# Optimization experiments

Measured on AMD Instinct MI355X. Metric: run time of the kernel, lower is better.

The kernel has to match this reference:

```python
import jax, jax.numpy as jnp
import numpy as np

CUTOFF = 5.2
BUCKETS_PER_CUTOFF = 1
BOX = 100.0
N_ATOMS = 100000
EXTRA_SPACE = 1e-5

# half-shell neighbor displacements: cartesian_prod(arange(-b,1)^3)[:-1] -> 7 vectors for b=1
_d1 = np.arange(-BUCKETS_PER_CUTOFF, 1)
DISPLACEMENTS = jnp.asarray(
    np.stack(np.meshgrid(_d1, _d1, _d1, indexing='ij'), axis=-1).reshape(-1, 3)[:-1],
    dtype=jnp.int32)  # (7, 3)
NUM_NEIGHBORS = DISPLACEMENTS.shape[0]


def setup_inputs() -> dict:
    key = jax.random.key(0)
    k1, _ = jax.random.split(key)
    # uniform in [0, 0.999*BOX) so fractional coordinates are strictly < 1
    coordinates = jax.random.uniform(k1, (1, N_ATOMS, 3), dtype=jnp.float32) * (BOX * 0.999)
    cell = jnp.eye(3, dtype=jnp.float32) * BOX
    return {"coordinates": coordinates, "cell": cell}


def _cumsum_from_zero(x):
    return jnp.concatenate([jnp.zeros((1,), x.dtype), jnp.cumsum(x[:-1])])


def reference(coordinates, cell):
    n_atoms = coordinates.shape[1]
    cell_diag = jnp.diagonal(cell)                       # (3,)
    bucket_length = CUTOFF / BUCKETS_PER_CUTOFF + EXTRA_SPACE
    grid = jnp.floor(cell_diag / bucket_length).astype(jnp.int32) + 1   # shape_buckets_grid (3,)
    total_buckets = int(grid[0] * grid[1] * grid[2])
    # faithful to source: [g1*g2, g1, 1]
    scaling = jnp.array([grid[1] * grid[2], grid[1], 1], dtype=jnp.int32)

    # fractionalize + main bucket vector/flat indices
    frac = coordinates / cell_diag.reshape(1, 1, -1)     # (1, N, 3)
    vec_idx = jnp.round(frac * (grid - 1).astype(frac.dtype)).astype(jnp.int32)  # (1, N, 3)
    flat = (vec_idx * scaling).sum(-1).reshape(-1)       # (N,) main_bucket_flat_index

    # image-index converters (stable argsort by bucket)
    imidx_from_atidx = jnp.argsort(flat)                 # jax argsort is stable
    atidx_from_imidx = jnp.argsort(imidx_from_atidx)

    # per-bucket counts / exclusive cumcounts
    counts = jnp.bincount(flat, length=total_buckets)
    cumcounts = _cumsum_from_zero(counts)
    max_in_bucket = int(counts.max())

    # ---- within-image pairs ----
    wp_idx = jnp.nonzero(counts > 1)[0]
    wp_count = counts[wp_idx]
    wp_cum = cumcounts[wp_idx]
    pu, pl = jnp.triu_indices(max_in_bucket, k=1)
    pairs = jnp.stack([pu, pl]).astype(jnp.int32)        # (2, P)
    # sort_along_row(row_for_sorting=1): key = upper + lower*max_in_bucket
    order = jnp.argsort(pairs[0] + pairs[1] * max_in_bucket)
    pairs = pairs[:, order]
    padded = pairs[None] + wp_cum.reshape(-1, 1, 1)      # (B, 2, P)
    padded = jnp.transpose(padded, (1, 0, 2)).reshape(2, -1)
    max_pairs = max_in_bucket * (max_in_bucket - 1) // 2
    mask = (jnp.arange(max_pairs)[None, :] < (wp_count * (wp_count - 1) // 2)[:, None]).reshape(-1)
    within_image_pairs = jnp.stack([padded[0][mask], padded[1][mask]])  # (2, n_pairs)

    # ---- between-image 'lower' indices ----
    neigh_vec = vec_idx[:, :, None, :] + DISPLACEMENTS   # (1, N, 7, 3)
    neigh_vec = jnp.mod(neigh_vec, grid)                 # pbc wrap of neighbor buckets
    neigh_flat = (neigh_vec * scaling).sum(-1)           # (1, N, 7)
    n_count = counts[neigh_flat]                         # (1, N, 7)
    n_cum = cumcounts[neigh_flat]                        # (1, N, 7)
    pad = jnp.broadcast_to(
        jnp.arange(max_in_bucket, dtype=n_cum.dtype).reshape(1, 1, 1, -1),
        (1, n_atoms, NUM_NEIGHBORS, max_in_bucket))      # (1, N, 7, M) -- dominant intermediate
    m = pad < n_count[..., None]
    lower_between = (pad + n_cum[..., None])[m]          # (n_between,)

    return within_image_pairs, lower_between, frac, imidx_from_atidx, atidx_from_imidx
```

## Files before the change

kernel.cpp:

```cpp
#include <hip/hip_runtime.h>
#include <hip/hip_bf16.h>

#define NB_MAX 8192
#define NTHR 256

__device__ __forceinline__ void get_grid(const float* __restrict__ cell,
                                         int& g0, int& g1, int& g2,
                                         float& d0, float& d1, float& d2) {
  d0 = cell[0]; d1 = cell[4]; d2 = cell[8];
  const float bl = (float)(5.2 + 1e-05);
  g0 = (int)floorf(d0 / bl) + 1;
  g1 = (int)floorf(d1 / bl) + 1;
  g2 = (int)floorf(d2 / bl) + 1;
}

__global__ void k_bucket_count(const float* __restrict__ coord,
                               const float* __restrict__ cell,
                               float* __restrict__ out_frac,
                               int* __restrict__ flat,
                               int* __restrict__ pv,
                               int* __restrict__ counts,
                               int* __restrict__ scalars, int n) {
  int a = blockIdx.x * blockDim.x + threadIdx.x;
  if (a >= n) return;
  int g0, g1, g2; float d0, d1, d2;
  get_grid(cell, g0, g1, g2, d0, d1, d2);
  if (a == 0) {
    scalars[8] = g0; scalars[9] = g1; scalars[10] = g2;
    scalars[11] = g1 * g2; scalars[12] = g0 * g1 * g2;
  }
  float x = coord[3 * a + 0], y = coord[3 * a + 1], z = coord[3 * a + 2];
  float fx = x / d0, fy = y / d1, fz = z / d2;
  out_frac[3 * a + 0] = fx;
  out_frac[3 * a + 1] = fy;
  out_frac[3 * a + 2] = fz;
  int v0 = (int)rintf(fx * (float)(g0 - 1));
  int v1 = (int)rintf(fy * (float)(g1 - 1));
  int v2 = (int)rintf(fz * (float)(g2 - 1));
  int b = v0 * (g1 * g2) + v1 * g1 + v2;
  flat[a] = b;
  pv[a] = (v0 << 20) | (v1 << 10) | v2;
  atomicAdd(&counts[b], 1);
}

__global__ __launch_bounds__(1024) void k_scan_buckets(
    const int* __restrict__ counts,
    int* __restrict__ cumc,
    int* __restrict__ pairoff,
    int* __restrict__ scalars) {
  int nb = scalars[12];
  const int T = 1024, IT = NB_MAX / 1024;
  __shared__ int wc[16], wp[16];
  int t = threadIdx.x;
  int lane = t & 63, wid = t >> 6;
  int base = t * IT;
  int cv[IT];
  int lc = 0, lp = 0;
  for (int i = 0; i < IT; ++i) {
    int idx = base + i;
    int c = (idx < nb) ? counts[idx] : 0;
    cv[i] = c;
    lc += c;
    lp += c * (c - 1) / 2;
  }
  int ic = lc, ip = lp;
  for (int off = 1; off < 64; off <<= 1) {
    int yc = __shfl_up(ic, off);
    int yp = __shfl_up(ip, off);
    if (lane >= off) { ic += yc; ip += yp; }
  }
  if (lane == 63) { wc[wid] = ic; wp[wid] = ip; }
  __syncthreads();
  if (wid == 0 && lane < 16) {
    int vc2 = wc[lane], vp2 = wp[lane];
    int sc2 = vc2, sp2 = vp2;
    for (int off = 1; off < 16; off <<= 1) {
      int yc = __shfl_up(sc2, off);
      int yp = __shfl_up(sp2, off);
      if (lane >= off) { sc2 += yc; sp2 += yp; }
    }
    wc[lane] = sc2 - vc2;
    wp[lane] = sp2 - vp2;
  }
  __syncthreads();
  int ec = wc[wid] + (ic - lc);
  int ep = wp[wid] + (ip - lp);
  for (int i = 0; i < IT; ++i) {
    int idx = base + i;
    if (idx < nb) { cumc[idx] = ec; pairoff[idx] = ep; }
    ec += cv[i];
    ep += cv[i] * (cv[i] - 1) / 2;
  }
  if (t == T - 1) scalars[0] = ep;
}

__global__ void k_scatter_runlen(const int* __restrict__ flat,
                                 const int* __restrict__ pv,
                                 const int* __restrict__ cumc,
                                 const int* __restrict__ counts,
                                 const int* __restrict__ scalars,
                                 int* __restrict__ fill,
                                 int* __restrict__ sorted,
                                 int* __restrict__ Oarr,
                                 int* __restrict__ blockpart, int n) {
  __shared__ int ws[4];
  int t = threadIdx.x;
  int lane = t & 63, wid = t >> 6;
  int a = blockIdx.x * NTHR + t;
  int S = 0;
  if (a < n) {
    int b = flat[a];
    int pos = cumc[b] + atomicAdd(&fill[b], 1);
    sorted[pos] = a;
    int g0 = scalars[8], g1 = scalars[9], g2 = scalars[10], g12 = scalars[11];
    int p = pv[a];
    int v0 = p >> 20, v1 = (p >> 10) & 1023, v2 = p & 1023;
#pragma unroll
    for (int m = 0; m < 7; ++m) {
      int dx = ((m >> 2) & 1) ? 0 : -1;
      int dy = ((m >> 1) & 1) ? 0 : -1;
      int dz = (m & 1) ? 0 : -1;
      int nx = v0 + dx; if (nx < 0) nx += g0;
      int ny = v1 + dy; if (ny < 0) ny += g1;
      int nz = v2 + dz; if (nz < 0) nz += g2;
      S += counts[nx * g12 + ny * g1 + nz];
    }
  }
  int iv = S;
  for (int off = 1; off < 64; off <<= 1) {
    int y = __shfl_up(iv, off);
    if (lane >= off) iv += y;
  }
  if (lane == 63) ws[wid] = iv;
  __syncthreads();
  if (wid == 0 && lane < 4) {
    int v2 = ws[lane], s2 = v2;
    for (int off = 1; off < 4; off <<= 1) {
      int y = __shfl_up(s2, off);
      if (lane >= off) s2 += y;
    }
    ws[lane] = s2 - v2;
    if (lane == 3) blockpart[blockIdx.x] = s2;
  }
  __syncthreads();
  if (a < n) Oarr[a] = ws[wid] + (iv - S);
}

__global__ void k_sort_perm_pairs(const int* __restrict__ counts,
                                  const int* __restrict__ cumc,
                                  const int* __restrict__ pairoff,
                                  const int* __restrict__ scalars,
                                  int* __restrict__ sorted,
                                  float* __restrict__ out_im,
                                  float* __restrict__ out_at,
                                  float* __restrict__ out,
                                  const int* __restrict__ blockpart,
                                  int* __restrict__ blockoff, int nblocks) {
  __shared__ int shm[4];
  int t = threadIdx.x;
  int lane = t & 63, wid = t >> 6;
  if (blockIdx.x == gridDim.x - 1) {
    int base = t * 4;
    int cv[4];
    int ls = 0;
    for (int i = 0; i < 4; ++i) {
      int v = (base + i < nblocks) ? blockpart[base + i] : 0;
      cv[i] = v;
      ls += v;
    }
    int il = ls;
    for (int off = 1; off < 64; off <<= 1) {
      int y = __shfl_up(il, off);
      if (lane >= off) il += y;
    }
    if (lane == 63) shm[wid] = il;
    __syncthreads();
    if (wid == 0 && lane < 4) {
      int v2 = shm[lane], s2 = v2;
      for (int off = 1; off < 4; off <<= 1) {
        int y = __shfl_up(s2, off);
        if (lane >= off) s2 += y;
      }
      shm[lane] = s2 - v2;
    }
    __syncthreads();
    int e = shm[wid] + (il - ls);
    for (int i = 0; i < 4; ++i) {
      blockoff[base + i] = e;
      e += cv[i];
    }
    return;
  }
  int b = blockIdx.x * 4 + wid;
  int nb = scalars[12];
  if (b >= nb) return;
  int c = counts[b];
  if (c == 0) return;
  int s = cumc[b];
  if (c == 1) {
    if (lane == 0) {
      int a = sorted[s];
      out_im[s] = (float)a;
      out_at[a] = (float)s;
    }
    return;
  }
  if (c <= 64) {
    int val = (lane < c) ? sorted[s + lane] : 0x7fffffff;
    int rank = 0;
    for (int j = 0; j < c; ++j) {
      int other = __shfl(val, j);
      rank += (other < val) ? 1 : 0;
    }
    if (lane < c) {
      sorted[s + rank] = val;
      out_im[s + rank] = (float)val;
      out_at[val] = (float)(s + rank);
    }
  } else if (lane == 0) {
    for (int i = 1; i < c; ++i) {
      int key = sorted[s + i];
      int j = i - 1;
      while (j >= 0 && sorted[s + j] > key) {
        sorted[s + j + 1] = sorted[s + j];
        --j;
      }
      sorted[s + j + 1] = key;
    }
    for (int i = 0; i < c; ++i) {
      int a = sorted[s + i];
      out_im[s + i] = (float)a;
      out_at[a] = (float)(s + i);
    }
  }
  int off = pairoff[b];
  int P = scalars[0];
  int np = c * (c - 1) / 2;
  for (int k = lane; k < np; k += 64) {
    int l = (int)((1.0f + sqrtf(1.0f + 8.0f * (float)k)) * 0.5f);
    while (l * (l - 1) / 2 > k) --l;
    while ((l + 1) * l / 2 <= k) ++l;
    int u = k - l * (l - 1) / 2;
    out[off + k] = (float)(s + u);
    out[P + off + k] = (float)(s + l);
  }
}

__global__ void k_emit16(const int* __restrict__ pv,
                         const int* __restrict__ counts,
                         const int* __restrict__ cumc,
                         const int* __restrict__ Oarr,
                         const int* __restrict__ blockoff,
                         const int* __restrict__ scalars,
                         float* __restrict__ out, int n) {
  int gt = blockIdx.x * blockDim.x + threadIdx.x;
  int a = gt >> 4;
  int l16 = gt & 15;
  if (a >= n) return;
  int g0 = scalars[8], g1 = scalars[9], g2 = scalars[10], g12 = scalars[11];
  int p = pv[a];
  int v0 = p >> 20, v1 = (p >> 10) & 1023, v2 = p & 1023;
  int segs[8];
  int cums[7];
  segs[0] = 0;
#pragma unroll
  for (int m = 0; m < 7; ++m) {
    int dx = ((m >> 2) & 1) ? 0 : -1;
    int dy = ((m >> 1) & 1) ? 0 : -1;
    int dz = (m & 1) ? 0 : -1;
    int nx = v0 + dx; if (nx < 0) nx += g0;
    int ny = v1 + dy; if (ny < 0) ny += g1;
    int nz = v2 + dz; if (nz < 0) nz += g2;
    int nb_ = nx * g12 + ny * g1 + nz;
    cums[m] = cumc[nb_];
    segs[m + 1] = segs[m] + counts[nb_];
  }
  int S = segs[7];
  long base = 2L * (long)scalars[0] + (long)blockoff[a >> 8] + (long)Oarr[a];
  for (int q = l16; q < S; q += 16) {
    int v = cums[0] + q;
#pragma unroll
    for (int m = 1; m < 7; ++m) {
      if (q >= segs[m]) v = cums[m] + (q - segs[m]);
    }
    out[base + q] = (float)v;
  }
}

extern "C" void kernel_launch(void* const* d_in, const int* in_sizes, int n_in,
                              void* d_out, int out_size, void* d_ws, size_t ws_size,
                              hipStream_t stream) {
  const float* coord = (const float*)d_in[0];
  const float* cell = (const float*)d_in[1];
  float* out = (float*)d_out;
  int n = in_sizes[0] / 3;

  int* W = (int*)d_ws;
  int* counts = W;
  int* fill = W + NB_MAX;
  int* scalars = W + 2 * NB_MAX;
  int* cumc = W + 2 * NB_MAX + 16;
  int* pairoff = cumc + NB_MAX;
  int* flat = pairoff + NB_MAX;
  int* pv = flat + n;
  int* sorted = pv + n;
  int* Oarr = sorted + n;
  int* blockpart = Oarr + n;
  int* blockoff = blockpart + 1024;

  float* out_frac = out + (out_size - 5 * n);
  float* out_im = out + (out_size - 2 * n);
  float* out_at = out + (out_size - n);

  int nblocks = (n + NTHR - 1) / NTHR;

  hipMemsetAsync(d_ws, 0, (size_t)(2 * NB_MAX + 16) * sizeof(int), stream);

  k_bucket_count<<<nblocks, NTHR, 0, stream>>>(coord, cell, out_frac, flat, pv, counts, scalars, n);
  k_scan_buckets<<<1, 1024, 0, stream>>>(counts, cumc, pairoff, scalars);
  k_scatter_runlen<<<nblocks, NTHR, 0, stream>>>(flat, pv, cumc, counts, scalars,
                                                 fill, sorted, Oarr, blockpart, n);
  k_sort_perm_pairs<<<NB_MAX / 4 + 1, 256, 0, stream>>>(counts, cumc, pairoff, scalars,
                                                        sorted, out_im, out_at, out,
                                                        blockpart, blockoff, nblocks);
  k_emit16<<<(n * 16 + 255) / 256, 256, 0, stream>>>(pv, counts, cumc, Oarr, blockoff,
                                                     scalars, out, n);
}
```

Before: 115.7 us.

## Fuse four pipeline kernels into one cooperative kernel with grid syncs

Replaces the bucket-count, bucket scan, scatter/run-length and sort/pair kernels with a single cooperative kernel that uses grid.sync between phases. The flat bucket index stays in a register instead of round-tripping through global memory, and the per-bucket sort phase becomes a grid-stride loop over warps. The aim is to remove launch overhead and inter-kernel gaps in a latency-bound pipeline. In exchange it adds grid-wide barrier cost, requires all ~391 blocks to be co-resident, and moves the bucket scan from a 1024-thread block to a single 256-thread block.

Measured after the change: 271.8 us. +135.0%, slower.

```diff
diff --git a/kernel.cpp b/kernel.cpp
--- a/kernel.cpp
+++ b/kernel.cpp
@@ -1,248 +1,227 @@
 #include <hip/hip_runtime.h>
 #include <hip/hip_bf16.h>
+#include <hip/hip_cooperative_groups.h>
+
+namespace cg = cooperative_groups;
 
 #define NB_MAX 8192
 #define NTHR 256
 
-__device__ __forceinline__ void get_grid(const float* __restrict__ cell,
-                                         int& g0, int& g1, int& g2,
-                                         float& d0, float& d1, float& d2) {
-  d0 = cell[0]; d1 = cell[4]; d2 = cell[8];
-  const float bl = (float)(5.2 + 1e-05);
-  g0 = (int)floorf(d0 / bl) + 1;
-  g1 = (int)floorf(d1 / bl) + 1;
-  g2 = (int)floorf(d2 / bl) + 1;
-}
-
-__global__ void k_bucket_count(const float* __restrict__ coord,
-                               const float* __restrict__ cell,
-                               float* __restrict__ out_frac,
-                               int* __restrict__ flat,
-                               int* __restrict__ pv,
-                               int* __restrict__ counts,
-                               int* __restrict__ scalars, int n) {
-  int a = blockIdx.x * blockDim.x + threadIdx.x;
-  if (a >= n) return;
-  int g0, g1, g2; float d0, d1, d2;
-  get_grid(cell, g0, g1, g2, d0, d1, d2);
-  if (a == 0) {
-    scalars[8] = g0; scalars[9] = g1; scalars[10] = g2;
-    scalars[11] = g1 * g2; scalars[12] = g0 * g1 * g2;
-  }
-  float x = coord[3 * a + 0], y = coord[3 * a + 1], z = coord[3 * a + 2];
-  float fx = x / d0, fy = y / d1, fz = z / d2;
-  out_frac[3 * a + 0] = fx;
-  out_frac[3 * a + 1] = fy;
-  out_frac[3 * a + 2] = fz;
-  int v0 = (int)rintf(fx * (float)(g0 - 1));
-  int v1 = (int)rintf(fy * (float)(g1 - 1));
-  int v2 = (int)rintf(fz * (float)(g2 - 1));
-  int b = v0 * (g1 * g2) + v1 * g1 + v2;
-  flat[a] = b;
-  pv[a] = (v0 << 20) | (v1 << 10) | v2;
-  atomicAdd(&counts[b], 1);
-}
-
-__global__ __launch_bounds__(1024) void k_scan_buckets(
-    const int* __restrict__ counts,
+__global__ __launch_bounds__(NTHR) void k_coop(
+    const float* __restrict__ coord,
+    const float* __restrict__ cell,
+    float* __restrict__ out_frac,
+    float* __restrict__ out_im,
+    float* __restrict__ out_at,
+    float* __restrict__ out,
+    int* __restrict__ pv,
+    int* __restrict__ counts,
+    int* __restrict__ fill,
+    int* __restrict__ scalars,
     int* __restrict__ cumc,
     int* __restrict__ pairoff,
-    int* __restrict__ scalars) {
-  int nb = scalars[12];
-  const int T = 1024, IT = NB_MAX / 1024;
-  __shared__ int wc[16], wp[16];
-  int t = threadIdx.x;
-  int lane = t & 63, wid = t >> 6;
-  int base = t * IT;
-  int cv[IT];
-  int lc = 0, lp = 0;
-  for (int i = 0; i < IT; ++i) {
-    int idx = base + i;
-    int c = (idx < nb) ? counts[idx] : 0;
-    cv[i] = c;
-    lc += c;
-    lp += c * (c - 1) / 2;
-  }
-  int ic = lc, ip = lp;
-  for (int off = 1; off < 64; off <<= 1) {
-    int yc = __shfl_up(ic, off);
-    int yp = __shfl_up(ip, off);
-    if (lane >= off) { ic += yc; ip += yp; }
-  }
-  if (lane == 63) { wc[wid] = ic; wp[wid] = ip; }
-  __syncthreads();
-  if (wid == 0 && lane < 16) {
-    int vc2 = wc[lane], vp2 = wp[lane];
-    int sc2 = vc2, sp2 = vp2;
-    for (int off = 1; off < 16; off <<= 1) {
-      int yc = __shfl_up(sc2, off);
-      int yp = __shfl_up(sp2, off);
-      if (lane >= off) { sc2 += yc; sp2 += yp; }
-    }
-    wc[lane] = sc2 - vc2;
-    wp[lane] = sp2 - vp2;
-  }
-  __syncthreads();
-  int ec = wc[wid] + (ic - lc);
-  int ep = wp[wid] + (ip - lp);
-  for (int i = 0; i < IT; ++i) {
-    int idx = base + i;
-    if (idx < nb) { cumc[idx] = ec; pairoff[idx] = ep; }
-    ec += cv[i];
-    ep += cv[i] * (cv[i] - 1) / 2;
-  }
-  if (t == T - 1) scalars[0] = ep;
-}
-
-__global__ void k_scatter_runlen(const int* __restrict__ flat,
-                                 const int* __restrict__ pv,
-                                 const int* __restrict__ cumc,
-                                 const int* __restrict__ counts,
-                                 const int* __restrict__ scalars,
-                                 int* __restrict__ fill,
-                                 int* __restrict__ sorted,
-                                 int* __restrict__ Oarr,
-                                 int* __restrict__ blockpart, int n) {
-  __shared__ int ws[4];
+    int* __restrict__ sorted,
+    int* __restrict__ Oarr,
+    int* __restrict__ blockpart,
+    int* __restrict__ blockoff,
+    int n) {
+  cg::grid_group grid = cg::this_grid();
+  __shared__ int shA[4], shB[4];
   int t = threadIdx.x;
   int lane = t & 63, wid = t >> 6;
   int a = blockIdx.x * NTHR + t;
-  int S = 0;
-  if (a < n) {
-    int b = flat[a];
-    int pos = cumc[b] + atomicAdd(&fill[b], 1);
-    sorted[pos] = a;
-    int g0 = scalars[8], g1 = scalars[9], g2 = scalars[10], g12 = scalars[11];
-    int p = pv[a];
-    int v0 = p >> 20, v1 = (p >> 10) & 1023, v2 = p & 1023;
+  bool active = a < n;
+
+  int flat_r = 0, pv_r = 0;
+  {
+    float d0 = cell[0], d1 = cell[4], d2 = cell[8];
+    const float bl = (float)(5.2 + 1e-05);
+    int g0 = (int)floorf(d0 / bl) + 1;
+    int g1 = (int)floorf(d1 / bl) + 1;
+    int g2 = (int)floorf(d2 / bl) + 1;
+    if (a == 0) {
+      scalars[8] = g0; scalars[9] = g1; scalars[10] = g2;
+      scalars[11] = g1 * g2; scalars[12] = g0 * g1 * g2;
+    }
+    if (active) {
+      float x = coord[3 * a + 0], y = coord[3 * a + 1], z = coord[3 * a + 2];
+      float fx = x / d0, fy = y / d1, fz = z / d2;
+      out_frac[3 * a + 0] = fx;
+      out_frac[3 * a + 1] = fy;
+      out_frac[3 * a + 2] = fz;
+      int v0 = (int)rintf(fx * (float)(g0 - 1));
+      int v1 = (int)rintf(fy * (float)(g1 - 1));
+      int v2 = (int)rintf(fz * (float)(g2 - 1));
+      flat_r = v0 * (g1 * g2) + v1 * g1 + v2;
+      pv_r = (v0 << 20) | (v1 << 10) | v2;
+      pv[a] = pv_r;
+      atomicAdd(&counts[flat_r], 1);
+    }
+  }
+  grid.sync();
+
+  if (blockIdx.x == 0) {
+    int nb = scalars[12];
+    const int IT = NB_MAX / NTHR;
+    int base2 = t * IT;
+    int lc = 0, lp = 0;
+    for (int i = 0; i < IT; ++i) {
+      int idx = base2 + i;
+      int c = (idx < nb) ? counts[idx] : 0;
+      lc += c;
+      lp += c * (c - 1) / 2;
+    }
+    int ic = lc, ip = lp;
+    for (int off = 1; off < 64; off <<= 1) {
+      int yc = __shfl_up(ic, off);
+      int yp = __shfl_up(ip, off);
+      if (lane >= off) { ic += yc; ip += yp; }
+    }
+    if (lane == 63) { shA[wid] = ic; shB[wid] = ip; }
+    __syncthreads();
+    if (wid == 0 && lane < 4) {
+      int vc2 = shA[lane], vp2 = shB[lane];
+      int sc2 = vc2, sp2 = vp2;
+      for (int off = 1; off < 4; off <<= 1) {
+        int yc = __shfl_up(sc2, off);
+        int yp = __shfl_up(sp2, off);
+        if (lane >= off) { sc2 += yc; sp2 += yp; }
+      }
+      shA[lane] = sc2 - vc2;
+      shB[lane] = sp2 - vp2;
+    }
+    __syncthreads();
+    int ec = shA[wid] + (ic - lc);
+    int ep = shB[wid] + (ip - lp);
+    for (int i = 0; i < IT; ++i) {
+      int idx = base2 + i;
+      int c = (idx < nb) ? counts[idx] : 0;
+      if (idx < nb) { cumc[idx] = ec; pairoff[idx] = ep; }
+      ec += c;
+      ep += c * (c - 1) / 2;
+    }
+    if (t == NTHR - 1) scalars[0] = ep;
+  }
+  grid.sync();
+
+  {
+    int S = 0;
+    if (active) {
+      int pos = cumc[flat_r] + atomicAdd(&fill[flat_r], 1);
+      sorted[pos] = a;
+      int g0 = scalars[8], g1 = scalars[9], g2 = scalars[10], g12 = scalars[11];
+      int v0 = pv_r >> 20, v1 = (pv_r >> 10) & 1023, v2 = pv_r & 1023;
 #pragma unroll
-    for (int m = 0; m < 7; ++m) {
-      int dx = ((m >> 2) & 1) ? 0 : -1;
-      int dy = ((m >> 1) & 1) ? 0 : -1;
-      int dz = (m & 1) ? 0 : -1;
-      int nx = v0 + dx; if (nx < 0) nx += g0;
-      int ny = v1 + dy; if (ny < 0) ny += g1;
-      int nz = v2 + dz; if (nz < 0) nz += g2;
-      S += counts[nx * g12 + ny * g1 + nz];
-    }
-  }
-  int iv = S;
-  for (int off = 1; off < 64; off <<= 1) {
-    int y = __shfl_up(iv, off);
-    if (lane >= off) iv += y;
-  }
-  if (lane == 63) ws[wid] = iv;
-  __syncthreads();
-  if (wid == 0 && lane < 4) {
-    int v2 = ws[lane], s2 = v2;
-    for (int off = 1; off < 4; off <<= 1) {
-      int y = __shfl_up(s2, off);
-      if (lane >= off) s2 += y;
-    }
-    ws[lane] = s2 - v2;
-    if (lane == 3) blockpart[blockIdx.x] = s2;
-  }
-  __syncthreads();
-  if (a < n) Oarr[a] = ws[wid] + (iv - S);
-}
-
-__global__ void k_sort_perm_pairs(const int* __restrict__ counts,
-                                  const int* __restrict__ cumc,
-                                  const int* __restrict__ pairoff,
-                                  const int* __restrict__ scalars,
-                                  int* __restrict__ sorted,
-                                  float* __restrict__ out_im,
-                                  float* __restrict__ out_at,
-                                  float* __restrict__ out,
-                                  const int* __restrict__ blockpart,
-                                  int* __restrict__ blockoff, int nblocks) {
-  __shared__ int shm[4];
-  int t = threadIdx.x;
-  int lane = t & 63, wid = t >> 6;
-  if (blockIdx.x == gridDim.x - 1) {
-    int base = t * 4;
-    int cv[4];
-    int ls = 0;
-    for (int i = 0; i < 4; ++i) {
-      int v = (base + i < nblocks) ? blockpart[base + i] : 0;
-      cv[i] = v;
-      ls += v;
-    }
-    int il = ls;
+      for (int m = 0; m < 7; ++m) {
+        int dx = ((m >> 2) & 1) ? 0 : -1;
+        int dy = ((m >> 1) & 1) ? 0 : -1;
+        int dz = (m & 1) ? 0 : -1;
+        int nx = v0 + dx; if (nx < 0) nx += g0;
+        int ny = v1 + dy; if (ny < 0) ny += g1;
+        int nz = v2 + dz; if (nz < 0) nz += g2;
+        S += counts[nx * g12 + ny * g1 + nz];
+      }
+    }
+    int iv = S;
     for (int off = 1; off < 64; off <<= 1) {
-      int y = __shfl_up(il, off);
-      if (lane >= off) il += y;
-    }
-    if (lane == 63) shm[wid] = il;
+      int y = __shfl_up(iv, off);
+      if (lane >= off) iv += y;
+    }
+    __syncthreads();
+    if (lane == 63) shA[wid] = iv;
     __syncthreads();
     if (wid == 0 && lane < 4) {
-      int v2 = shm[lane], s2 = v2;
+      int v2 = shA[lane], s2 = v2;
       for (int off = 1; off < 4; off <<= 1) {
         int y = __shfl_up(s2, off);
         if (lane >= off) s2 += y;
       }
-      shm[lane] = s2 - v2;
-    }
-    __syncthreads();
-    int e = shm[wid] + (il - ls);
-    for (int i = 0; i < 4; ++i) {
-      blockoff[base + i] = e;
-      e += cv[i];
-    }
-    return;
-  }
-  int b = blockIdx.x * 4 + wid;
-  int nb = scalars[12];
-  if (b >= nb) return;
-  int c = counts[b];
-  if (c == 0) return;
-  int s = cumc[b];
-  if (c == 1) {
-    if (lane == 0) {
-      int a = sorted[s];
-      out_im[s] = (float)a;
-      out_at[a] = (float)s;
-    }
-    return;
-  }
-  if (c <= 64) {
-    int val = (lane < c) ? sorted[s + lane] : 0x7fffffff;
-    int rank = 0;
-    for (int j = 0; j < c; ++j) {
-      int other = __shfl(val, j);
-      rank += (other < val) ? 1 : 0;
-    }
-    if (lane < c) {
-      sorted[s + rank] = val;
-      out_im[s + rank] = (float)val;
-      out_at[val] = (float)(s + rank);
-    }
-  } else if (lane == 0) {
-    for (int i = 1; i < c; ++i) {
-      int key = sorted[s + i];
-      int j = i - 1;
-      while (j >= 0 && sorted[s + j] > key) {
-        sorted[s + j + 1] = sorted[s + j];
-        --j;
-      }
-      sorted[s + j + 1] = key;
-    }
-    for (int i = 0; i < c; ++i) {
-      int a = sorted[s + i];
-      out_im[s + i] = (float)a;
-      out_at[a] = (float)(s + i);
-    }
-  }
-  int off = pairoff[b];
-  int P = scalars[0];
-  int np = c * (c - 1) / 2;
-  for (int k = lane; k < np; k += 64) {
-    int l = (int)((1.0f + sqrtf(1.0f + 8.0f * (float)k)) * 0.5f);
-    while (l * (l - 1) / 2 > k) --l;
-    while ((l + 1) * l / 2 <= k) ++l;
-    int u = k - l * (l - 1) / 2;
-    out[off + k] = (float)(s + u);
-    out[P + off + k] = (float)(s + l);
+      shA[lane] = s2 - v2;
+      if (lane == 3) blockpart[blockIdx.x] = s2;
+    }
+    __syncthreads();
+    if (active) Oarr[a] = shA[wid] + (iv - S);
+  }
+  grid.sync();
+
+  {
+    int gw = blockIdx.x * 4 + wid;
+    int nwaves = gridDim.x * 4;
+    int nblocks = gridDim.x;
+    if (gw == 0) {
+      int cv[7];
+      int ls = 0;
+      for (int i = 0; i < 7; ++i) {
+        int idx = lane * 7 + i;
+        int v = (idx < nblocks) ? blockpart[idx] : 0;
+        cv[i] = v;
+        ls += v;
+      }
+      int il = ls;
+      for (int off = 1; off < 64; off <<= 1) {
+        int y = __shfl_up(il, off);
+        if (lane >= off) il += y;
+      }
+      int e = il - ls;
+      for (int i = 0; i < 7; ++i) {
+        int idx = lane * 7 + i;
+        if (idx < nblocks) blockoff[idx] = e;
+        e += cv[i];
+      }
+    }
+    int nb = scalars[12];
+    int P = scalars[0];
+    for (int b = gw; b < nb; b += nwaves) {
+      int c = counts[b];
+      if (c == 0) continue;
+      int s = cumc[b];
+      if (c == 1) {
+        if (lane == 0) {
+          int aa = sorted[s];
+          out_im[s] = (float)aa;
+          out_at[aa] = (float)s;
+        }
+        continue;
+      }
+      if (c <= 64) {
+        int val = (lane < c) ? sorted[s + lane] : 0x7fffffff;
+        int rank = 0;
+        for (int j = 0; j < c; ++j) {
+          int other = __shfl(val, j);
+          rank += (other < val) ? 1 : 0;
+        }
+        if (lane < c) {
+          sorted[s + rank] = val;
+          out_im[s + rank] = (float)val;
+          out_at[val] = (float)(s + rank);
+        }
+      } else if (lane == 0) {
+        for (int i = 1; i < c; ++i) {
+          int key = sorted[s + i];
+          int j = i - 1;
+          while (j >= 0 && sorted[s + j] > key) {
+            sorted[s + j + 1] = sorted[s + j];
+            --j;
+          }
+          sorted[s + j + 1] = key;
+        }
+        for (int i = 0; i < c; ++i) {
+          int aa = sorted[s + i];
+          out_im[s + i] = (float)aa;
+          out_at[aa] = (float)(s + i);
+        }
+      }
+      int off = pairoff[b];
+      int np = c * (c - 1) / 2;
+      for (int k = lane; k < np; k += 64) {
+        int l = (int)((1.0f + sqrtf(1.0f + 8.0f * (float)k)) * 0.5f);
+        while (l * (l - 1) / 2 > k) --l;
+        while ((l + 1) * l / 2 <= k) ++l;
+        int u = k - l * (l - 1) / 2;
+        out[off + k] = (float)(s + u);
+        out[P + off + k] = (float)(s + l);
+      }
+    }
   }
 }
 
@@ -301,8 +280,7 @@
   int* scalars = W + 2 * NB_MAX;
   int* cumc = W + 2 * NB_MAX + 16;
   int* pairoff = cumc + NB_MAX;
-  int* flat = pairoff + NB_MAX;
-  int* pv = flat + n;
+  int* pv = pairoff + NB_MAX;
   int* sorted = pv + n;
   int* Oarr = sorted + n;
   int* blockpart = Oarr + n;
@@ -316,13 +294,14 @@
 
   hipMemsetAsync(d_ws, 0, (size_t)(2 * NB_MAX + 16) * sizeof(int), stream);
 
-  k_bucket_count<<<nblocks, NTHR, 0, stream>>>(coord, cell, out_frac, flat, pv, counts, scalars, n);
-  k_scan_buckets<<<1, 1024, 0, stream>>>(counts, cumc, pairoff, scalars);
-  k_scatter_runlen<<<nblocks, NTHR, 0, stream>>>(flat, pv, cumc, counts, scalars,
-                                                 fill, sorted, Oarr, blockpart, n);
-  k_sort_perm_pairs<<<NB_MAX / 4 + 1, 256, 0, stream>>>(counts, cumc, pairoff, scalars,
-                                                        sorted, out_im, out_at, out,
-                                                        blockpart, blockoff, nblocks);
+  void* kargs[] = {
+      (void*)&coord, (void*)&cell, (void*)&out_frac, (void*)&out_im,
+      (void*)&out_at, (void*)&out, (void*)&pv, (void*)&counts,
+      (void*)&fill, (void*)&scalars, (void*)&cumc, (void*)&pairoff,
+      (void*)&sorted, (void*)&Oarr, (void*)&blockpart, (void*)&blockoff,
+      (void*)&n};
+  hipLaunchCooperativeKernel((void*)k_coop, dim3(nblocks), dim3(NTHR), kargs, 0, stream);
+
   k_emit16<<<(n * 16 + 255) / 256, 256, 0, stream>>>(pv, counts, cumc, Oarr, blockoff,
                                                      scalars, out, n);
 }
```
